# Performance work log

Measured on AMD Instinct MI355X. Metric: run time of the kernel, lower is better.

## Reference

```python
import jax, jax.numpy as jnp
import numpy as np

B, N, L = 2, 2048, 2048
DQ, DKV, H, WF = 1024, 1024, 16, 4
HD = DQ // H
EPS = 1e-5


def _ln(x, g, b):
    m = jnp.mean(x, axis=-1, keepdims=True)
    v = jnp.mean(jnp.square(x - m), axis=-1, keepdims=True)
    return (x - m) * jax.lax.rsqrt(v + EPS) * g + b


def setup_inputs() -> dict:
    key = jax.random.key(0)
    ks = jax.random.split(key, 12)
    s = 0.02
    return {
        "x_q": jax.random.normal(ks[0], (B, N, DQ), jnp.float32),
        "x_kv": jax.random.normal(ks[1], (B, L, DKV), jnp.float32),
        "qn_g": jnp.ones((DQ,), jnp.float32),
        "qn_b": jnp.zeros((DQ,), jnp.float32),
        "kvn_g": jnp.ones((DKV,), jnp.float32),
        "kvn_b": jnp.zeros((DKV,), jnp.float32),
        "Wq": jax.random.normal(ks[2], (DQ, DQ), jnp.float32) * s,
        "bq": jnp.zeros((DQ,), jnp.float32),
        "Wk": jax.random.normal(ks[3], (DQ, DKV), jnp.float32) * s,
        "bk": jnp.zeros((DQ,), jnp.float32),
        "Wv": jax.random.normal(ks[4], (DQ, DKV), jnp.float32) * s,
        "bv": jnp.zeros((DQ,), jnp.float32),
        "Wo": jax.random.normal(ks[5], (DQ, DQ), jnp.float32) * s,
        "bo": jnp.zeros((DQ,), jnp.float32),
        "n2_g": jnp.ones((DQ,), jnp.float32),
        "n2_b": jnp.zeros((DQ,), jnp.float32),
        "W1": jax.random.normal(ks[6], (WF * DQ, DQ), jnp.float32) * s,
        "b1": jnp.zeros((WF * DQ,), jnp.float32),
        "W2": jax.random.normal(ks[7], (DQ, WF * DQ), jnp.float32) * s,
        "b2": jnp.zeros((DQ,), jnp.float32),
    }


def reference(x_q, x_kv, qn_g, qn_b, kvn_g, kvn_b, Wq, bq, Wk, bk, Wv, bv,
              Wo, bo, n2_g, n2_b, W1, b1, W2, b2):
    # projections (torch Linear: x @ W.T + b)
    q = (_ln(x_q, qn_g, qn_b) @ Wq.T + bq).reshape(B, N, H, HD)
    kvn = _ln(x_kv, kvn_g, kvn_b)
    k = (kvn @ Wk.T + bk).reshape(B, L, H, HD)
    v = (kvn @ Wv.T + bv).reshape(B, L, H, HD)

    # attention with softmax-1: exp(s)/(1 + sum exp(s)), numerically stable
    scale = 1.0 / jnp.sqrt(jnp.float32(HD))
    s = jnp.einsum("bnhd,blhd->bhnl", q, k) * scale  # [B,H,N,L]
    m = jnp.max(s, axis=-1, keepdims=True)
    m = jnp.maximum(m, 0.0)  # include the implicit zero logit of softmax-1
    p = jnp.exp(s - m)
    denom = jnp.sum(p, axis=-1, keepdims=True) + jnp.exp(-m)
    attn = p / denom
    attn_out = jnp.einsum("bhnl,blhd->bnhd", attn, v).reshape(B, N, DQ)

    # residual + out proj
    x = x_q + (attn_out @ Wo.T + bo)
    # residual MLP (GELU, exact/erf as torch nn.GELU default)
    h = jax.nn.gelu(_ln(x, n2_g, n2_b) @ W1.T + b1, approximate=False)
    x = x + (h @ W2.T + b2)
    return x
```

## Files before the change

kernel.cpp:

```cpp
#include <hip/hip_runtime.h>
#include <hip/hip_bf16.h>
#include <stdint.h>

#define DEV __device__ __forceinline__

typedef unsigned short ushort_t;
typedef __attribute__((ext_vector_type(8))) short bf16x8;
typedef __attribute__((ext_vector_type(4))) float f32x4;

DEV uint32_t f2bf2(float lo, float hi) {
  uint32_t d;
  asm("v_cvt_pk_bf16_f32 %0, %1, %2" : "=v"(d) : "v"(lo), "v"(hi));
  return d;
}
DEV ushort_t f2bf(float f) { return (ushort_t)f2bf2(f, f); }

DEV void gload_lds16(const void* gp, void* lp) {
  __builtin_amdgcn_global_load_lds(
      (__attribute__((address_space(1))) void*)(void*)(uintptr_t)gp,
      (__attribute__((address_space(3))) void*)lp, 16, 0, 0);
}

DEV float gelu_fast(float x) {
  const float z = fabsf(x) * 0.70710678118654752f;
  const float t = __builtin_amdgcn_rcpf(fmaf(0.3275911f, z, 1.0f));
  float p = fmaf(1.061405429f, t, -1.453152027f);
  p = fmaf(p, t, 1.421413741f);
  p = fmaf(p, t, -0.284496736f);
  p = fmaf(p, t, 0.254829592f);
  p *= t;
  const float e = __builtin_amdgcn_exp2f(z * z * -1.4426950408889634f);
  const float er = fmaf(-p, e, 1.0f);
  const float s = copysignf(er, x);
  return 0.5f * x * (1.0f + s);
}

DEV void ln_row(const float* __restrict__ x, const float* __restrict__ g,
                const float* __restrict__ be, ushort_t* __restrict__ out, int row) {
  const int t = threadIdx.x;
  const float4 v = ((const float4*)(x + (size_t)row * 1024))[t];
  float s = v.x + v.y + v.z + v.w;
  float sq = v.x * v.x + v.y * v.y + v.z * v.z + v.w * v.w;
#pragma unroll
  for (int d = 1; d < 64; d <<= 1) { s += __shfl_xor(s, d); sq += __shfl_xor(sq, d); }
  __shared__ float sm[8];
  const int w = t >> 6, lane = t & 63;
  if (lane == 0) { sm[w * 2] = s; sm[w * 2 + 1] = sq; }
  __syncthreads();
  s = sm[0] + sm[2] + sm[4] + sm[6];
  sq = sm[1] + sm[3] + sm[5] + sm[7];
  const float mean = s * (1.f / 1024.f);
  const float var = sq * (1.f / 1024.f) - mean * mean;
  const float rstd = rsqrtf(var + 1e-5f);
  const float4 gv = ((const float4*)g)[t];
  const float4 bv = ((const float4*)be)[t];
  uint2 o;
  o.x = f2bf2((v.x - mean) * rstd * gv.x + bv.x, (v.y - mean) * rstd * gv.y + bv.y);
  o.y = f2bf2((v.z - mean) * rstd * gv.z + bv.z, (v.w - mean) * rstd * gv.w + bv.w);
  ((uint2*)(out + (size_t)row * 1024))[t] = o;
}

__global__ __launch_bounds__(256) void cvt_ln(
    const float* __restrict__ Wq, const float* __restrict__ Wk,
    const float* __restrict__ Wv, const float* __restrict__ Wo,
    const float* __restrict__ W1, const float* __restrict__ W2,
    ushort_t* __restrict__ WQKVB, ushort_t* __restrict__ WoB,
    ushort_t* __restrict__ W1B, ushort_t* __restrict__ W2B,
    const float* __restrict__ x_q, const float* __restrict__ x_kv,
    const float* __restrict__ qg, const float* __restrict__ qb,
    const float* __restrict__ kg, const float* __restrict__ kb,
    ushort_t* __restrict__ oq, ushort_t* __restrict__ okv) {
  if (blockIdx.x < 12288) {
    int i = blockIdx.x * 256 + threadIdx.x;
    const float* src; ushort_t* dst; int j;
    if (i < 262144)            { src = Wq; dst = WQKVB;            j = i; }
    else if (i < 524288)       { src = Wk; dst = WQKVB + 1048576;  j = i - 262144; }
    else if (i < 786432)       { src = Wv; dst = WQKVB + 2097152;  j = i - 524288; }
    else if (i < 1048576)      { src = Wo; dst = WoB;              j = i - 786432; }
    else if (i < 2097152)      { src = W1; dst = W1B;              j = i - 1048576; }
    else                       { src = W2; dst = W2B;              j = i - 2097152; }
    float4 v = ((const float4*)src)[j];
    uint2 o; o.x = f2bf2(v.x, v.y); o.y = f2bf2(v.z, v.w);
    ((uint2*)dst)[j] = o;
  } else {
    const int r = blockIdx.x - 12288;
    if (r < 4096) ln_row(x_q, qg, qb, oq, r);
    else ln_row(x_kv, kg, kb, okv, r - 4096);
  }
}

__global__ __launch_bounds__(256) void ln_bf16(const float* __restrict__ x,
                                               const float* __restrict__ g,
                                               const float* __restrict__ be,
                                               ushort_t* __restrict__ out) {
  ln_row(x, g, be, out, blockIdx.x);
}

DEV void xcd_remap(int gx, int gy, int& bx, int& by) {
  const int lin = by * gx + bx;
  const int xcd = lin & 7, s = lin >> 3;
  by = xcd * (gy >> 3) + s / gx;
  bx = s % gx;
}

enum { EPI_BF16 = 0, EPI_KV = 1, EPI_RESID = 2, EPI_GELU = 3, EPI_QKV = 4 };

template <int BM, int TN, int BK, int EPI>
__global__ __launch_bounds__(256, (BM == 64) ? 4 : 3) void gemm_bt(
    const ushort_t* __restrict__ A,
    const ushort_t* __restrict__ A2,
    const ushort_t* __restrict__ Wb,
    const float* __restrict__ bias, const float* __restrict__ bias2,
    const float* __restrict__ bias3,
    const float* __restrict__ resid,
    void* __restrict__ outp, void* __restrict__ outp2, void* __restrict__ outp3,
    int M, int N, int K, float oscale) {
  constexpr int WAVES_N = (TN == 128 || BM == 64) ? 2 : 1;
  constexpr int WAVES_M = 4 / WAVES_N;
  constexpr int NI = BM / WAVES_M / 16;
  constexpr int NJ = TN / WAVES_N / 16;
  constexpr int CH = BK / 8;
  constexpr int NA = (BM * CH) / 256;
  constexpr int NBL = (TN * CH) / 256;
  constexpr int KS = BK / 32;
  __shared__ ushort_t As[2][BM * BK];
  __shared__ ushort_t Bs[2][TN * BK];
  const int t = threadIdx.x;
  const int w = t >> 6, lane = t & 63;
  const int qd = lane >> 4, ql = lane & 15;
  int bx = blockIdx.x, by = blockIdx.y;
  xcd_remap(gridDim.x, gridDim.y, bx, by);
  const int m0 = by * BM, n0 = bx * TN;
  const int wm = (w / WAVES_N) * (BM / WAVES_M);
  const int wn = (w % WAVES_N) * (TN / WAVES_N);
  const int sw = (BK == 64) ? (ql & 7) : ((ql >> 1) & 3);

  const ushort_t* Ause = (EPI == EPI_QKV && n0 >= 1024) ? A2 : A;

  const ushort_t* pa[NA];
#pragma unroll
  for (int p = 0; p < NA; p++) {
    int n = p * 256 + t, row = n / CH, c = n % CH;
    int g = (BK == 64) ? (c ^ (row & 7)) : (c ^ ((row >> 1) & 3));
    pa[p] = Ause + (size_t)(m0 + row) * K + g * 8;
  }
  const ushort_t* pb[NBL];
#pragma unroll
  for (int p = 0; p < NBL; p++) {
    int n = p * 256 + t, row = n / CH, c = n % CH;
    int g = (BK == 64) ? (c ^ (row & 7)) : (c ^ ((row >> 1) & 3));
    pb[p] = Wb + (size_t)(n0 + row) * K + g * 8;
  }

#pragma unroll
  for (int p = 0; p < NA; p++) { gload_lds16(pa[p], &As[0][(p * 256 + t) * 8]); pa[p] += BK; }
#pragma unroll
  for (int p = 0; p < NBL; p++) { gload_lds16(pb[p], &Bs[0][(p * 256 + t) * 8]); pb[p] += BK; }
  __syncthreads();

  f32x4 acc[NI][NJ] = {};
  const int NIT = K / BK;
  int cur = 0;

  for (int it = 0; it < NIT; ++it) {
    if (it + 1 < NIT) {
#pragma unroll
      for (int p = 0; p < NA; p++) { gload_lds16(pa[p], &As[1 ^ cur][(p * 256 + t) * 8]); pa[p] += BK; }
#pragma unroll
      for (int p = 0; p < NBL; p++) { gload_lds16(pb[p], &Bs[1 ^ cur][(p * 256 + t) * 8]); pb[p] += BK; }
    }
    const ushort_t* Ac = As[cur];
    const ushort_t* Bc = Bs[cur];
#pragma unroll
    for (int ks = 0; ks < KS; ks++) {
      bf16x8 af[NI], bf[NJ];
#pragma unroll
      for (int i = 0; i < NI; i++)
        af[i] = *(const bf16x8*)&Ac[(wm + i * 16 + ql) * BK + ((ks * 4 + qd) ^ sw) * 8];
#pragma unroll
      for (int j = 0; j < NJ; j++)
        bf[j] = *(const bf16x8*)&Bc[(wn + j * 16 + ql) * BK + ((ks * 4 + qd) ^ sw) * 8];
#pragma unroll
      for (int i = 0; i < NI; i++)
#pragma unroll
        for (int j = 0; j < NJ; j++)
          acc[i][j] = __builtin_amdgcn_mfma_f32_16x16x32_bf16(af[i], bf[j], acc[i][j], 0, 0, 0);
    }
    __syncthreads();
    cur ^= 1;
  }

#pragma unroll
  for (int i = 0; i < NI; i++) {
    const int mr = m0 + wm + i * 16 + qd * 4;
#pragma unroll
    for (int j = 0; j < NJ; j++) {
      const int col = n0 + wn + j * 16 + ql;
      f32x4 v = acc[i][j];
      if constexpr (EPI == EPI_BF16) {
        const float bb = bias[col];
        ushort_t* o = (ushort_t*)outp;
#pragma unroll
        for (int r = 0; r < 4; r++) o[(size_t)(mr + r) * N + col] = f2bf((v[r] + bb) * oscale);
      } else if constexpr (EPI == EPI_QKV) {
        if (col < 1024) {
          const float bb = bias[col];
          ushort_t* o = (ushort_t*)outp;
#pragma unroll
          for (int r = 0; r < 4; r++) o[(size_t)(mr + r) * 1024 + col] = f2bf((v[r] + bb) * oscale);
        } else if (col < 2048) {
          const int c2 = col - 1024;
          const float bb = bias2[c2];
          ushort_t* o = (ushort_t*)outp2;
#pragma unroll
          for (int r = 0; r < 4; r++) o[(size_t)(mr + r) * 1024 + c2] = f2bf(v[r] + bb);
        } else {
          const int vc = col - 2048;
          const float bb = bias3[vc];
          const int h = vc >> 6, d = vc & 63;
          const int b = mr >> 11, l0 = mr & 2047;
          uint2 pk;
          pk.x = f2bf2(v[0] + bb, v[1] + bb);
          pk.y = f2bf2(v[2] + bb, v[3] + bb);
          *(uint2*)((ushort_t*)outp3 + ((((size_t)b * 16 + h) * 64 + d) * 2048 + l0)) = pk;
        }
      } else if constexpr (EPI == EPI_RESID) {
        const float bb = bias[col];
        float* o = (float*)outp;
#pragma unroll
        for (int r = 0; r < 4; r++) {
          size_t idx = (size_t)(mr + r) * N + col;
          o[idx] = resid[idx] + v[r] + bb;
        }
      } else if constexpr (EPI == EPI_GELU) {
        const float bb = bias[col];
        ushort_t* o = (ushort_t*)outp;
#pragma unroll
        for (int r = 0; r < 4; r++)
          o[(size_t)(mr + r) * N + col] = f2bf(gelu_fast(v[r] + bb));
      }
    }
  }
}

__global__ __launch_bounds__(256, 2) void flash_attn(const ushort_t* __restrict__ Qg,
                                                     const ushort_t* __restrict__ Kg,
                                                     const ushort_t* __restrict__ VTg,
                                                     ushort_t* __restrict__ Og) {
  __shared__ ushort_t QPs[128 * 64];
  __shared__ ushort_t Ks[2][64 * 64];
  __shared__ ushort_t Vs[2][64 * 64];
  const int t = threadIdx.x, w = t >> 6, lane = t & 63;
  const int qd = lane >> 4, ql = lane & 15;
  int bx = blockIdx.x, bh = blockIdx.y;
  xcd_remap(gridDim.x, gridDim.y, bx, bh);
  const int b = bh >> 4, h = bh & 15;
  const int n0 = bx * 128;
  const ushort_t* Qp = Qg + ((size_t)b * 2048 + n0) * 1024 + h * 64;
  const ushort_t* Kp = Kg + (size_t)b * 2048 * 1024 + h * 64;
  const ushort_t* Vp = VTg + (size_t)bh * 64 * 2048;
  const int sw = ql & 7;

  const ushort_t* kp2[2];
  const ushort_t* vp2[2];
#pragma unroll
  for (int p = 0; p < 2; p++) {
    int n = p * 256 + t, row = n >> 3, c = (n & 7) ^ (row & 7);
    kp2[p] = Kp + (size_t)row * 1024 + c * 8;
    vp2[p] = Vp + (size_t)row * 2048 + c * 8;
  }

#pragma unroll
  for (int p = 0; p < 4; p++) {
    int n = p * 256 + t, row = n >> 3, c = (n & 7) ^ (row & 7);
    gload_lds16(Qp + (size_t)row * 1024 + c * 8, &QPs[n * 8]);
  }
#pragma unroll
  for (int p = 0; p < 2; p++) {
    int n = p * 256 + t;
    gload_lds16(kp2[p], &Ks[0][n * 8]);
    gload_lds16(vp2[p], &Vs[0][n * 8]);
    kp2[p] += 64 * 1024;
    vp2[p] += 64;
  }
  __syncthreads();

  bf16x8 aq[2][2];
#pragma unroll
  for (int i = 0; i < 2; i++)
#pragma unroll
    for (int ks = 0; ks < 2; ks++)
      aq[i][ks] = *(const bf16x8*)&QPs[(w * 32 + i * 16 + ql) * 64 + ((ks * 4 + qd) ^ sw) * 8];
  __syncthreads();

  f32x4 accO[2][4] = {};
  float lro2[2] = {0.f, 0.f};

  int cur = 0;
  for (int lt = 0; lt < 32; ++lt) {
    if (lt + 1 < 32) {
#pragma unroll
      for (int p = 0; p < 2; p++) {
        int n = p * 256 + t;
        gload_lds16(kp2[p], &Ks[1 ^ cur][n * 8]);
        gload_lds16(vp2[p], &Vs[1 ^ cur][n * 8]);
        kp2[p] += 64 * 1024;
        vp2[p] += 64;
      }
    }
    const ushort_t* Kc = Ks[cur];
    const ushort_t* Vc = Vs[cur];

    f32x4 accS[4][2] = {};
#pragma unroll
    for (int ks = 0; ks < 2; ks++) {
      bf16x8 bk[4];
#pragma unroll
      for (int j = 0; j < 4; j++)
        bk[j] = *(const bf16x8*)&Kc[(j * 16 + ql) * 64 + ((ks * 4 + qd) ^ sw) * 8];
      __builtin_amdgcn_s_setprio(1);
#pragma unroll
      for (int j = 0; j < 4; j++)
#pragma unroll
        for (int i = 0; i < 2; i++)
          accS[j][i] = __builtin_amdgcn_mfma_f32_16x16x32_bf16(bk[j], aq[i][ks], accS[j][i], 0, 0, 0);
      __builtin_amdgcn_s_setprio(0);
    }

#pragma unroll
    for (int j = 0; j < 4; j++)
#pragma unroll
      for (int i = 0; i < 2; i++) {
        f32x4 p;
#pragma unroll
        for (int r = 0; r < 4; r++) {
          p[r] = __builtin_amdgcn_exp2f(accS[j][i][r]);
          lro2[i] += p[r];
        }
        const int n = w * 32 + i * 16 + ql;
        const int coff = (((j * 2 + (qd >> 1)) ^ sw) << 3) + ((qd & 1) << 2);
        uint2 pk; pk.x = f2bf2(p[0], p[1]); pk.y = f2bf2(p[2], p[3]);
        *(uint2*)&QPs[n * 64 + coff] = pk;
      }

#pragma unroll
    for (int ks = 0; ks < 2; ks++) {
      bf16x8 ap[2], bv[4];
#pragma unroll
      for (int i = 0; i < 2; i++)
        ap[i] = *(const bf16x8*)&QPs[(w * 32 + i * 16 + ql) * 64 + ((ks * 4 + qd) ^ sw) * 8];
#pragma unroll
      for (int jo = 0; jo < 4; jo++)
        bv[jo] = *(const bf16x8*)&Vc[(jo * 16 + ql) * 64 + ((ks * 4 + qd) ^ sw) * 8];
      __builtin_amdgcn_s_setprio(1);
#pragma unroll
      for (int i = 0; i < 2; i++)
#pragma unroll
        for (int jo = 0; jo < 4; jo++)
          accO[i][jo] = __builtin_amdgcn_mfma_f32_16x16x32_bf16(ap[i], bv[jo], accO[i][jo], 0, 0, 0);
      __builtin_amdgcn_s_setprio(0);
    }

    __syncthreads();
    cur ^= 1;
  }

  float dn[2];
#pragma unroll
  for (int i = 0; i < 2; i++) {
    float l = lro2[i];
    l += __shfl_xor(l, 16);
    l += __shfl_xor(l, 32);
    dn[i] = l + 1.0f;
  }

#pragma unroll
  for (int i = 0; i < 2; i++)
#pragma unroll
    for (int r = 0; r < 4; r++) {
      const float inv = 1.0f / __shfl(dn[i], qd * 4 + r);
      const int row = n0 + w * 32 + i * 16 + qd * 4 + r;
#pragma unroll
      for (int jo = 0; jo < 4; jo++)
        Og[((size_t)b * 2048 + row) * 1024 + h * 64 + jo * 16 + ql] =
            f2bf(accO[i][jo][r] * inv);
    }
}

extern "C" void kernel_launch(void* const* d_in, const int* in_sizes, int n_in,
                              void* d_out, int out_size, void* d_ws, size_t ws_size,
                              hipStream_t stream) {
  const float* x_q = (const float*)d_in[0];
  const float* x_kv = (const float*)d_in[1];
  const float* qn_g = (const float*)d_in[2];
  const float* qn_b = (const float*)d_in[3];
  const float* kvn_g = (const float*)d_in[4];
  const float* kvn_b = (const float*)d_in[5];
  const float* Wq = (const float*)d_in[6];
  const float* bq = (const float*)d_in[7];
  const float* Wk = (const float*)d_in[8];
  const float* bk = (const float*)d_in[9];
  const float* Wv = (const float*)d_in[10];
  const float* bv = (const float*)d_in[11];
  const float* Wo = (const float*)d_in[12];
  const float* bo = (const float*)d_in[13];
  const float* n2_g = (const float*)d_in[14];
  const float* n2_b = (const float*)d_in[15];
  const float* W1 = (const float*)d_in[16];
  const float* b1 = (const float*)d_in[17];
  const float* W2 = (const float*)d_in[18];
  const float* b2 = (const float*)d_in[19];

  char* ws = (char*)d_ws;
  const size_t MB = 1ull << 20;
  ushort_t* WQKVB = (ushort_t*)(ws + 0 * MB);
  ushort_t* WoB = (ushort_t*)(ws + 6 * MB);
  ushort_t* W1B = (ushort_t*)(ws + 8 * MB);
  ushort_t* W2B = (ushort_t*)(ws + 16 * MB);
  ushort_t* LNQ = (ushort_t*)(ws + 24 * MB);
  ushort_t* LNKV = (ushort_t*)(ws + 32 * MB);
  ushort_t* Qb = (ushort_t*)(ws + 40 * MB);
  ushort_t* Kb = (ushort_t*)(ws + 48 * MB);
  ushort_t* VTb = (ushort_t*)(ws + 56 * MB);
  ushort_t* AOb = (ushort_t*)(ws + 64 * MB);
  float* Xf = (float*)(ws + 72 * MB);
  ushort_t* LN2 = (ushort_t*)(ws + 88 * MB);
  ushort_t* Hb = (ushort_t*)(ws + 24 * MB);

  const float QSCALE = 0.18033688011112042f;

  cvt_ln<<<20480, 256, 0, stream>>>(Wq, Wk, Wv, Wo, W1, W2, WQKVB, WoB, W1B, W2B,
                                    x_q, x_kv, qn_g, qn_b, kvn_g, kvn_b, LNQ, LNKV);

  gemm_bt<128, 128, 32, EPI_QKV><<<dim3(24, 32), 256, 0, stream>>>(
      LNQ, LNKV, WQKVB, bq, bk, bv, nullptr, Qb, Kb, VTb, 4096, 3072, 1024, QSCALE);

  flash_attn<<<dim3(16, 32), 256, 0, stream>>>(Qb, Kb, VTb, AOb);

  gemm_bt<64, 64, 64, EPI_RESID><<<dim3(16, 64), 256, 0, stream>>>(
      AOb, nullptr, WoB, bo, nullptr, nullptr, x_q, Xf, nullptr, nullptr,
      4096, 1024, 1024, 1.0f);
  ln_bf16<<<4096, 256, 0, stream>>>(Xf, n2_g, n2_b, LN2);
  gemm_bt<128, 128, 32, EPI_GELU><<<dim3(32, 32), 256, 0, stream>>>(
      LN2, nullptr, W1B, b1, nullptr, nullptr, nullptr, Hb, nullptr, nullptr,
      4096, 4096, 1024, 1.0f);
  gemm_bt<64, 64, 64, EPI_RESID><<<dim3(16, 64), 256, 0, stream>>>(
      Hb, nullptr, W2B, b2, nullptr, nullptr, Xf, (float*)d_out, nullptr, nullptr,
      4096, 1024, 4096, 1.0f);
}
```

Before: 354.8 us.

## Add 256x256-tile 512-thread bf16 GEMM for the GELU MLP up-projection

Adds a new GEMM kernel that uses 256x256 output tiles, 512 threads (8 waves in a 2x4 arrangement) and a K-step of 64. It double-buffers LDS with direct global-to-LDS loads and splits each K-step into four MFMA phases separated by barriers, raising wave priority around the MFMA blocks. It replaces the 128x128 gemm_bt for the 4096x4096x1024 W1 projection with GELU epilogue. The goal is more data reuse per LDS load and fewer blocks. The cost is about 128KB of LDS per block, so only one block fits per CU, and the 256-block grid is roughly a single wave.

```diff
diff --git a/kernel.cpp b/kernel.cpp
--- a/kernel.cpp
+++ b/kernel.cpp
@@ -243,6 +243,121 @@
   }
 }
 
+template <int EPI>
+__global__ __launch_bounds__(512, 2) void gemm256v2(
+    const ushort_t* __restrict__ A, const ushort_t* __restrict__ Wb,
+    const float* __restrict__ bias,
+    void* __restrict__ outp, int M, int N, int K, float oscale) {
+  __shared__ ushort_t As[2][256 * 64];
+  __shared__ ushort_t Bs[2][256 * 64];
+  const int t = threadIdx.x;
+  const int w = t >> 6, lane = t & 63;
+  const int qd = lane >> 4, ql = lane & 15;
+  const int wr = w >> 2, wc = w & 3;
+  int bx = blockIdx.x, by = blockIdx.y;
+  xcd_remap(gridDim.x, gridDim.y, bx, by);
+  const int m0 = by * 256, n0 = bx * 256;
+  const int sw = ql & 7;
+
+  const ushort_t* pa[4];
+  const ushort_t* pb[4];
+#pragma unroll
+  for (int p = 0; p < 4; p++) {
+    const int n = p * 512 + t, row = n >> 3, c = (n & 7) ^ (row & 7);
+    pa[p] = A + (size_t)(m0 + row) * K + c * 8;
+    pb[p] = Wb + (size_t)(n0 + row) * K + c * 8;
+  }
+
+#pragma unroll
+  for (int p = 0; p < 4; p++) { gload_lds16(pa[p], &As[0][(p * 512 + t) * 8]); pa[p] += 64; }
+#pragma unroll
+  for (int p = 0; p < 4; p++) { gload_lds16(pb[p], &Bs[0][(p * 512 + t) * 8]); pb[p] += 64; }
+  __syncthreads();
+
+  f32x4 acc[8][4] = {};
+  const int NT = K / 64;
+  int cur = 0;
+
+#define AFREAD(KS)                                                              \
+  _Pragma("unroll") for (int i = 0; i < 8; i++)                                 \
+      af[i] = *(const bf16x8*)&Ac[(wr * 128 + i * 16 + ql) * 64 +               \
+                                  (((KS) * 4 + qd) ^ sw) * 8];
+#define BFREAD(KS, NH)                                                          \
+  _Pragma("unroll") for (int jj = 0; jj < 2; jj++)                              \
+      bf[jj] = *(const bf16x8*)&Bc[(wc * 64 + (NH) * 32 + jj * 16 + ql) * 64 +  \
+                                   (((KS) * 4 + qd) ^ sw) * 8];
+#define MM(NH)                                                                  \
+  __builtin_amdgcn_s_setprio(1);                                                \
+  _Pragma("unroll") for (int i = 0; i < 8; i++)                                 \
+      _Pragma("unroll") for (int jj = 0; jj < 2; jj++)                          \
+          acc[i][(NH) * 2 + jj] = __builtin_amdgcn_mfma_f32_16x16x32_bf16(      \
+              af[i], bf[jj], acc[i][(NH) * 2 + jj], 0, 0, 0);                   \
+  __builtin_amdgcn_s_setprio(0);
+
+  for (int T = 0; T < NT; ++T) {
+    const ushort_t* Ac = As[cur];
+    const ushort_t* Bc = Bs[cur];
+    ushort_t* An = As[cur ^ 1];
+    ushort_t* Bn = Bs[cur ^ 1];
+    const bool st = (T + 1 < NT);
+    bf16x8 af[8], bf[2];
+
+    if (st) {
+#pragma unroll
+      for (int p = 0; p < 4; p++) { gload_lds16(pa[p], &An[(p * 512 + t) * 8]); pa[p] += 64; }
+#pragma unroll
+      for (int p = 0; p < 4; p++) { gload_lds16(pb[p], &Bn[(p * 512 + t) * 8]); pb[p] += 64; }
+    }
+    AFREAD(0)
+    BFREAD(0, 0)
+    MM(0)
+    __builtin_amdgcn_s_barrier();
+
+    BFREAD(0, 1)
+    MM(1)
+    __builtin_amdgcn_s_barrier();
+
+    AFREAD(1)
+    BFREAD(1, 0)
+    MM(0)
+    __builtin_amdgcn_s_barrier();
+
+    BFREAD(1, 1)
+    MM(1)
+    if (st) asm volatile("s_waitcnt vmcnt(0)" ::: "memory");
+    __builtin_amdgcn_sched_barrier(0);
+    __builtin_amdgcn_s_barrier();
+    __builtin_amdgcn_sched_barrier(0);
+    cur ^= 1;
+  }
+#undef AFREAD
+#undef BFREAD
+#undef MM
+
+#pragma unroll
+  for (int i = 0; i < 8; i++) {
+    const int mr = m0 + wr * 128 + i * 16 + qd * 4;
+#pragma unroll
+    for (int j = 0; j < 4; j++) {
+      const int col = n0 + wc * 64 + j * 16 + ql;
+      f32x4 v = acc[i][j];
+      if constexpr (EPI == EPI_GELU) {
+        const float bb = bias[col];
+        ushort_t* o = (ushort_t*)outp;
+#pragma unroll
+        for (int r = 0; r < 4; r++)
+          o[(size_t)(mr + r) * N + col] = f2bf(gelu_fast(v[r] + bb));
+      } else if constexpr (EPI == EPI_BF16) {
+        const float bb = bias[col];
+        ushort_t* o = (ushort_t*)outp;
+#pragma unroll
+        for (int r = 0; r < 4; r++)
+          o[(size_t)(mr + r) * N + col] = f2bf((v[r] + bb) * oscale);
+      }
+    }
+  }
+}
+
 __global__ __launch_bounds__(256, 2) void flash_attn(const ushort_t* __restrict__ Qg,
                                                      const ushort_t* __restrict__ Kg,
                                                      const ushort_t* __restrict__ VTg,
@@ -441,9 +556,8 @@
       AOb, nullptr, WoB, bo, nullptr, nullptr, x_q, Xf, nullptr, nullptr,
       4096, 1024, 1024, 1.0f);
   ln_bf16<<<4096, 256, 0, stream>>>(Xf, n2_g, n2_b, LN2);
-  gemm_bt<128, 128, 32, EPI_GELU><<<dim3(32, 32), 256, 0, stream>>>(
-      LN2, nullptr, W1B, b1, nullptr, nullptr, nullptr, Hb, nullptr, nullptr,
-      4096, 4096, 1024, 1.0f);
+  gemm256v2<EPI_GELU><<<dim3(16, 16), 512, 0, stream>>>(
+      LN2, W1B, b1, Hb, 4096, 4096, 1024, 1.0f);
   gemm_bt<64, 64, 64, EPI_RESID><<<dim3(16, 64), 256, 0, stream>>>(
       Hb, nullptr, W2B, b2, nullptr, nullptr, Xf, (float*)d_out, nullptr, nullptr,
       4096, 1024, 4096, 1.0f);
```

Result: no change. 354.3 us, median of 2 (-0.1%).
